# Kernel tuning notes

Measured on AMD Instinct MI355X. Metric: run time of the kernel, lower is better.

Reference implementation:

```python
import jax, jax.numpy as jnp
import numpy as np

B, IMG, C = 128, 128, 3
NP = 8                      # n_patches per side
PS = IMG // NP              # patch size = 16
IN_D = C * PS * PS          # 768
E, NH, L, A = 768, 12, 12, 256
HS = E // NH                # 64
T = NP * NP + 1             # 65 tokens (cls + patches)
LN_EPS = 1e-5


def _pos_emb(seq_len, d):
    i = np.arange(seq_len, dtype=np.float64)[:, None]
    j = np.arange(d, dtype=np.float64)[None, :]
    even = np.sin(i / 10000 ** (j / d))
    odd = np.cos(i / 10000 ** ((j - 1) / d))
    return jnp.asarray(np.where(j % 2 == 0, even, odd), dtype=jnp.float32)


def setup_inputs() -> dict:
    key = jax.random.key(0)
    ks = jax.random.split(key, 16)
    s_e = 1.0 / np.sqrt(E)
    s_in = 1.0 / np.sqrt(IN_D)
    s_4e = 1.0 / np.sqrt(4 * E)
    return {
        "images": jax.random.normal(ks[0], (B, IMG, IMG, C), jnp.float32),
        "lin_w": jax.random.normal(ks[1], (IN_D, E), jnp.float32) * s_in,
        "cls_tok": jax.random.uniform(ks[2], (1, E), jnp.float32),
        "pos_emb": _pos_emb(T, E),
        "Wq": jax.random.normal(ks[3], (L, E, E), jnp.float32) * s_e,
        "Wk": jax.random.normal(ks[4], (L, E, E), jnp.float32) * s_e,
        "Wv": jax.random.normal(ks[5], (L, E, E), jnp.float32) * s_e,
        "Wo": jax.random.normal(ks[6], (L, E, E), jnp.float32) * s_e,
        "bo": jnp.zeros((L, E), jnp.float32),
        "ln1g": jnp.ones((L, E), jnp.float32),
        "ln1b": jnp.zeros((L, E), jnp.float32),
        "ln2g": jnp.ones((L, E), jnp.float32),
        "ln2b": jnp.zeros((L, E), jnp.float32),
        "W1": jax.random.normal(ks[7], (L, E, 4 * E), jnp.float32) * s_e,
        "b1": jnp.zeros((L, 4 * E), jnp.float32),
        "W2": jax.random.normal(ks[8], (L, 4 * E, E), jnp.float32) * s_4e,
        "b2": jnp.zeros((L, E), jnp.float32),
        "head_w": jax.random.normal(ks[9], (E, A), jnp.float32) * s_e,
        "head_b": jnp.zeros((A,), jnp.float32),
    }


def _layernorm(x, g, b):
    mu = jnp.mean(x, axis=-1, keepdims=True)
    var = jnp.var(x, axis=-1, keepdims=True)
    return (x - mu) * jax.lax.rsqrt(var + LN_EPS) * g + b


def _vit_forward(images, lin_w, cls_tok, pos_emb, Wq, Wk, Wv, Wo, bo,
                 ln1g, ln1b, ln2g, ln2b, W1, b1, W2, b2, head_w, head_b):
    n = images.shape[0]
    # patches: 'b (h p1) (w p2) c -> b (h w) (p1 p2 c)'
    p = images.reshape(n, NP, PS, NP, PS, C)
    patches = p.transpose(0, 1, 3, 2, 4, 5).reshape(n, NP * NP, IN_D)
    x = patches @ lin_w                                   # [B, 64, E]
    x = jnp.concatenate([jnp.broadcast_to(cls_tok, (n, 1, E)), x], axis=1)
    x = x + pos_emb[None]                                 # [B, T, E]

    scale = E ** (-0.5)  # NOTE: original scales by n_embd, not head_size

    def block(x, params):
        wq, wk, wv, wo_, bo_, g1, be1, g2, be2, w1, bb1, w2, bb2 = params
        h = _layernorm(x, g1, be1)
        q = (h @ wq).reshape(n, T, NH, HS)
        k = (h @ wk).reshape(n, T, NH, HS)
        v = (h @ wv).reshape(n, T, NH, HS)
        wei = jnp.einsum('bthd,bshd->bhts', q, k) * scale
        wei = jax.nn.softmax(wei, axis=-1)
        attn = jnp.einsum('bhts,bshd->bthd', wei, v).reshape(n, T, E)
        x = x + attn @ wo_ + bo_
        h2 = _layernorm(x, g2, be2)
        x = x + jax.nn.relu(h2 @ w1 + bb1) @ w2 + bb2
        return x, None

    x, _ = jax.lax.scan(block, x,
                        (Wq, Wk, Wv, Wo, bo, ln1g, ln1b, ln2g, ln2b,
                         W1, b1, W2, b2))
    cls = x[:, 0]                                          # [B, E]
    logits = jax.nn.softmax(cls @ head_w + head_b, axis=-1)  # model ends in Softmax
    return logits


def reference(images, lin_w, cls_tok, pos_emb, Wq, Wk, Wv, Wo, bo,
              ln1g, ln1b, ln2g, ln2b, W1, b1, W2, b2, head_w, head_b):
    return _vit_forward(images, lin_w, cls_tok, pos_emb, Wq, Wk, Wv, Wo, bo,
                        ln1g, ln1b, ln2g, ln2b, W1, b1, W2, b2, head_w, head_b)
```

## Files before the change

### kernel.cpp

```cpp
#include <hip/hip_runtime.h>
#include <cstdint>
#include <cstddef>


typedef __bf16 bf16x8 __attribute__((ext_vector_type(8)));
typedef float  f32x4  __attribute__((ext_vector_type(4)));

#define DEVINL __device__ __forceinline__

DEVINL uint16_t f2bf(float f){
  union U{float f; uint32_t i;} v; v.f=f; uint32_t u=v.i;
  return (uint16_t)((u + 0x7fffu + ((u>>16)&1u)) >> 16);
}

DEVINL void gl_lds16(const void* g, void* l){
  __builtin_amdgcn_global_load_lds((const __attribute__((address_space(1))) void*)g,
                                   (__attribute__((address_space(3))) void*)l, 16, 0, 0);
}

__global__ __launch_bounds__(256) void patchify_k(const float* __restrict__ img,
                                                  uint16_t* __restrict__ out){
  int i = blockIdx.x*256 + threadIdx.x;
  int m  = i / 768, kk = i - m*768;
  int b  = m >> 6,  t  = m & 63;
  int py = t >> 3,  px = t & 7;
  int r  = kk / 48, rem = kk - r*48;
  size_t src = ((size_t)(b*128 + py*16 + r)*128 + px*16)*3 + rem;
  out[i] = f2bf(img[src]);
}

DEVINL void tile_transpose(const float* __restrict__ src, uint16_t* __restrict__ dst,
                           int R, int C, int ti, int tj, int tid){
  __shared__ uint16_t tile[32][33];
  int tx = tid & 31, ty = tid >> 5;
  int r0 = ti*32, c0 = tj*32;
  #pragma unroll
  for (int i=0;i<4;++i)
    tile[ty+i*8][tx] = f2bf(src[(size_t)(r0+ty+i*8)*C + c0 + tx]);
  __syncthreads();
  #pragma unroll
  for (int i=0;i<4;++i)
    dst[(size_t)(c0+ty+i*8)*R + r0 + tx] = tile[tx][ty+i*8];
}

__global__ __launch_bounds__(256) void transpose_cvt_k(const float* __restrict__ src,
                                                       uint16_t* __restrict__ dst, int R, int C){
  tile_transpose(src, dst, R, C, blockIdx.y, blockIdx.x, threadIdx.x);
}

__global__ __launch_bounds__(256) void prep_layer_k(
    const float* __restrict__ Wq, const float* __restrict__ Wk,
    const float* __restrict__ Wv, const float* __restrict__ Wo,
    const float* __restrict__ W1, const float* __restrict__ W2,
    uint16_t* __restrict__ wbuf){
  int idx = blockIdx.x;
  const float* src; uint16_t* dst; int R, C, ti, tj;
  if (idx < 2304){
    int m = idx / 576, t = idx - m*576; ti = t/24; tj = t - ti*24; R=768; C=768;
    src = (m==0)?Wq:(m==1)?Wk:(m==2)?Wv:Wo;
    dst = wbuf + (size_t)m*589824;
  } else if (idx < 4608){
    int t = idx - 2304; ti = t/96; tj = t - ti*96; R=768; C=3072;
    src = W1; dst = wbuf + 2359296;
  } else {
    int t = idx - 4608; ti = t/24; tj = t - ti*24; R=3072; C=768;
    src = W2; dst = wbuf + 4718592;
  }
  tile_transpose(src, dst, R, C, ti, tj, threadIdx.x);
}

__global__ __launch_bounds__(256) void cls_init_k(const float* __restrict__ ct,
                                                  const float* __restrict__ pos,
                                                  float* __restrict__ X){
  int b = blockIdx.x, tid = threadIdx.x;
  for (int e = tid; e < 768; e += 256)
    X[(size_t)b*65*768 + e] = ct[e] + pos[e];
}

__global__ __launch_bounds__(256) void ln_k(const float* __restrict__ Xin,
                                            uint16_t* __restrict__ H,
                                            const float* __restrict__ g,
                                            const float* __restrict__ b){
  int row = blockIdx.x, tid = threadIdx.x;
  const float* xr = Xin + (size_t)row*768;
  float v0 = xr[tid], v1 = xr[tid+256], v2 = xr[tid+512];
  int wid = tid>>6, lane = tid&63;
  __shared__ float part[4];
  __shared__ float bc[2];
  float s = v0+v1+v2;
  #pragma unroll
  for (int o=32;o;o>>=1) s += __shfl_down(s,o);
  if (lane==0) part[wid] = s;
  __syncthreads();
  if (tid==0) bc[0] = (part[0]+part[1]+part[2]+part[3]) * (1.f/768.f);
  __syncthreads();
  float mu = bc[0];
  float d0=v0-mu, d1=v1-mu, d2=v2-mu;
  float q = d0*d0 + d1*d1 + d2*d2;
  #pragma unroll
  for (int o=32;o;o>>=1) q += __shfl_down(q,o);
  __syncthreads();
  if (lane==0) part[wid] = q;
  __syncthreads();
  if (tid==0) bc[1] = rsqrtf((part[0]+part[1]+part[2]+part[3])*(1.f/768.f) + 1e-5f);
  __syncthreads();
  float rs = bc[1];
  uint16_t* hr = H + (size_t)row*768;
  hr[tid]     = f2bf(d0*rs*g[tid]     + b[tid]);
  hr[tid+256] = f2bf(d1*rs*g[tid+256] + b[tid+256]);
  hr[tid+512] = f2bf(d2*rs*g[tid+512] + b[tid+512]);
}

enum { EP_BF16=0, EP_RES=1, EP_RELU=2, EP_EMB=3 };

template<int MODE, int BN>
__global__ __launch_bounds__(256) void gemm_bt_k(
    const uint16_t* __restrict__ A, const uint16_t* __restrict__ Bt,
    int M, int N, int K, int strideB, long long strideO,
    const float* __restrict__ bias, float* __restrict__ X,
    uint16_t* __restrict__ Obf, const float* __restrict__ pos)
{
  constexpr int WN = BN/2;
  constexpr int NF = WN/16;
  constexpr int BLOADS = BN/64;
  __shared__ __align__(16) uint16_t sA[3][128*32];
  __shared__ __align__(16) uint16_t sB[3][BN*32];
  const int tid = threadIdx.x;
  const int wid = tid>>6, lane = tid&63;
  const int nx = gridDim.x;
  const int nwg = nx*gridDim.y;
  int idx = blockIdx.y*nx + blockIdx.x;
  int q8 = nwg>>3, r8 = nwg&7, xcd = idx&7, off = idx>>3;
  int swz = (xcd<r8 ? xcd*(q8+1) : r8*(q8+1) + (xcd-r8)*q8) + off;
  const int bn = (swz % nx)*BN, bm = (swz / nx)*128;
  const int z = blockIdx.z;
  const uint16_t* Bz = Bt + (size_t)z*strideB;
  const int wr = wid>>1, wc = wid&1;
  const int frow = lane&15, g = lane>>4;
  int srA[2], scA[2];
  #pragma unroll
  for (int rr=0; rr<2; ++rr){
    int G = rr*256 + tid;
    srA[rr] = G>>2; scA[rr] = ((G&3) - (G>>3)) & 3;
  }
  int srB[BLOADS], scB[BLOADS];
  #pragma unroll
  for (int rr=0; rr<BLOADS; ++rr){
    int G = rr*256 + tid;
    srB[rr] = G>>2; scB[rr] = ((G&3) - (G>>3)) & 3;
  }
  const int rsw = (frow>>1)&3;
  f32x4 acc[4][NF] = {};
  const int nt = K>>5;

  auto stage = [&](char* dA, char* dB, int k0){
    #pragma unroll
    for (int rr=0; rr<2; ++rr)
      gl_lds16(A + (size_t)(bm+srA[rr])*K + k0 + scA[rr]*8, dA + (rr*256 + wid*64)*16);
    #pragma unroll
    for (int rr=0; rr<BLOADS; ++rr)
      gl_lds16(Bz + (size_t)(bn+srB[rr])*K + k0 + scB[rr]*8, dB + (rr*256 + wid*64)*16);
  };

  char *cA=(char*)sA[0], *nA=(char*)sA[1], *fA=(char*)sA[2];
  char *cB=(char*)sB[0], *nB=(char*)sB[1], *fB=(char*)sB[2];
  stage(cA, cB, 0);
  stage(nA, nB, 32);

  for (int t = 0; t < nt; ++t){
    if (t+2 < nt){
      stage(fA, fB, (t+2)<<5);
      if constexpr (BLOADS==1) asm volatile("s_waitcnt vmcnt(6)" ::: "memory");
      else                     asm volatile("s_waitcnt vmcnt(8)" ::: "memory");
    } else if (t+1 < nt){
      if constexpr (BLOADS==1) asm volatile("s_waitcnt vmcnt(3)" ::: "memory");
      else                     asm volatile("s_waitcnt vmcnt(4)" ::: "memory");
    } else {
      asm volatile("s_waitcnt vmcnt(0)" ::: "memory");
    }
    __builtin_amdgcn_s_barrier();
    bf16x8 a[4], b[NF];
    #pragma unroll
    for (int m=0;m<4;++m)
      a[m] = *(const bf16x8*)(cA + (wr*64+m*16+frow)*64 + (((g+rsw)&3)<<4));
    #pragma unroll
    for (int n=0;n<NF;++n)
      b[n] = *(const bf16x8*)(cB + (wc*WN+n*16+frow)*64 + (((g+rsw)&3)<<4));
    #pragma unroll
    for (int m=0;m<4;++m)
      #pragma unroll
      for (int n=0;n<NF;++n)
        acc[m][n] = __builtin_amdgcn_mfma_f32_16x16x32_bf16(a[m], b[n], acc[m][n], 0,0,0);
    __builtin_amdgcn_s_barrier();
    char* t1=cA; cA=nA; nA=fA; fA=t1;
    char* t2=cB; cB=nB; nB=fB; fB=t2;
  }

  uint16_t* Oz = Obf + (size_t)z*(size_t)strideO;
  #pragma unroll
  for (int m=0;m<4;++m){
    int gr0 = bm + wr*64 + m*16 + (lane>>4)*4;
    #pragma unroll
    for (int n=0;n<NF;++n){
      int gc = bn + wc*WN + n*16 + (lane&15);
      #pragma unroll
      for (int r=0;r<4;++r){
        int grow = gr0 + r;
        float vsum = acc[m][n][r];
        if constexpr (MODE==EP_BF16){
          Oz[(size_t)grow*N + gc] = f2bf(vsum);
        } else if constexpr (MODE==EP_RES){
          X[(size_t)grow*N + gc] += vsum + bias[gc];
        } else if constexpr (MODE==EP_RELU){
          float u = vsum + bias[gc];
          Oz[(size_t)grow*N + gc] = f2bf(u > 0.f ? u : 0.f);
        } else {
          int t2i = grow & 63, bb = grow >> 6;
          X[((size_t)bb*65 + 1 + t2i)*768 + gc] = vsum + pos[(size_t)(t2i+1)*768 + gc];
        }
      }
    }
  }
}

__global__ __launch_bounds__(320) void attn_mfma_k(const uint16_t* __restrict__ q,
    const uint16_t* __restrict__ k, const uint16_t* __restrict__ v,
    uint16_t* __restrict__ o)
{
  __shared__ __align__(16) uint16_t P_lds[80][104];
  __shared__ __align__(16) uint16_t Vt[64][104];
  const int bh = blockIdx.x; const int b = bh / 12, hd = bh - b*12;
  const int tid = threadIdx.x;
  const int m = tid>>6;
  const int lane = tid&63;
  const int g = lane>>4, c = lane&15;
  const size_t base = (size_t)b*65*768 + (size_t)hd*64;

  for (int i = tid; i < 80*16; i += 320) P_lds[i>>4][80 + (i&15)] = 0;
  for (int i = tid; i < 64*32; i += 320) Vt[i>>5][64 + (i&31)] = 0;
  __syncthreads();
  for (int j = tid; j < 520; j += 320){
    int key = j >> 3, dc = j & 7;
    union { bf16x8 v8; uint16_t u[8]; } gv;
    gv.v8 = *(const bf16x8*)&v[base + (size_t)key*768 + dc*8];
    #pragma unroll
    for (int e = 0; e < 8; ++e) Vt[dc*8 + e][key] = gv.u[e];
  }

  bf16x8 bk[5][2];
  #pragma unroll
  for (int n=0;n<5;++n)
    #pragma unroll
    for (int kk=0;kk<2;++kk)
      bk[n][kk] = *(const bf16x8*)&k[base + (size_t)(n*16 + c)*768 + kk*32 + g*8];

  bf16x8 aq[2];
  #pragma unroll
  for (int kk=0;kk<2;++kk)
    aq[kk] = *(const bf16x8*)&q[base + (size_t)(m*16 + c)*768 + kk*32 + g*8];
  f32x4 sacc[5] = {};
  #pragma unroll
  for (int kk=0;kk<2;++kk)
    #pragma unroll
    for (int n=0;n<5;++n)
      sacc[n] = __builtin_amdgcn_mfma_f32_16x16x32_bf16(aq[kk], bk[n][kk], sacc[n], 0,0,0);

  const float scale = 0.03608439182435161f;
  #pragma unroll
  for (int r=0;r<4;++r){
    float val[5]; float mx = -3.0e38f;
    #pragma unroll
    for (int n=0;n<5;++n){
      val[n] = (n*16 + c) < 65 ? sacc[n][r]*scale : -3.0e38f;
      mx = fmaxf(mx, val[n]);
    }
    #pragma unroll
    for (int off=1; off<16; off<<=1) mx = fmaxf(mx, __shfl_xor(mx, off));
    float p[5], sum = 0.f;
    #pragma unroll
    for (int n=0;n<5;++n){
      p[n] = (n*16 + c) < 65 ? __expf(val[n]-mx) : 0.f;
      sum += p[n];
    }
    #pragma unroll
    for (int off=1; off<16; off<<=1) sum += __shfl_xor(sum, off);
    float rinv = 1.f / sum;
    int row = m*16 + g*4 + r;
    #pragma unroll
    for (int n=0;n<5;++n) P_lds[row][n*16 + c] = f2bf(p[n]*rinv);
  }
  __syncthreads();

  bf16x8 vb[4][3];
  #pragma unroll
  for (int n=0;n<4;++n)
    #pragma unroll
    for (int kk=0;kk<3;++kk)
      vb[n][kk] = *(const bf16x8*)&Vt[n*16 + c][kk*32 + g*8];
  f32x4 oacc[4] = {};
  #pragma unroll
  for (int kk=0;kk<3;++kk){
    bf16x8 pa = *(const bf16x8*)&P_lds[m*16 + c][kk*32 + g*8];
    #pragma unroll
    for (int n=0;n<4;++n)
      oacc[n] = __builtin_amdgcn_mfma_f32_16x16x32_bf16(pa, vb[n][kk], oacc[n], 0,0,0);
  }
  #pragma unroll
  for (int r=0;r<4;++r){
    int row = m*16 + g*4 + r;
    if (row < 65){
      #pragma unroll
      for (int n=0;n<4;++n)
        o[base + (size_t)row*768 + n*16 + c] = f2bf(oacc[n][r]);
    }
  }
}

__global__ __launch_bounds__(256) void head_k(const float* __restrict__ X,
    const float* __restrict__ W, const float* __restrict__ bias,
    float* __restrict__ out){
  int b = blockIdx.x, a = threadIdx.x;
  const float* xr = X + (size_t)b*65*768;
  float acc = bias[a];
  for (int kk=0; kk<768; ++kk) acc += xr[kk]*W[(size_t)kk*256 + a];
  int wid = a>>6, lane = a&63;
  __shared__ float red[4];
  float mx = acc;
  #pragma unroll
  for (int off=32; off; off>>=1) mx = fmaxf(mx, __shfl_xor(mx, off));
  if (lane==0) red[wid]=mx;
  __syncthreads();
  mx = fmaxf(fmaxf(red[0],red[1]), fmaxf(red[2],red[3]));
  float e = __expf(acc-mx);
  float s = e;
  #pragma unroll
  for (int off=32; off; off>>=1) s += __shfl_xor(s, off);
  __syncthreads();
  if (lane==0) red[wid]=s;
  __syncthreads();
  s = red[0]+red[1]+red[2]+red[3];
  out[(size_t)b*256 + a] = e/s;
}

extern "C" void kernel_launch(void* const* d_in, const int* in_sizes, int n_in,
                              void* d_out, int out_size, void* d_ws, size_t ws_size,
                              hipStream_t stream)
{
  const float* images = (const float*)d_in[0];
  const float* lin_w  = (const float*)d_in[1];
  const float* cls_tok= (const float*)d_in[2];
  const float* pos    = (const float*)d_in[3];
  const float* Wq = (const float*)d_in[4];
  const float* Wk = (const float*)d_in[5];
  const float* Wv = (const float*)d_in[6];
  const float* Wo = (const float*)d_in[7];
  const float* bo = (const float*)d_in[8];
  const float* ln1g=(const float*)d_in[9];
  const float* ln1b=(const float*)d_in[10];
  const float* ln2g=(const float*)d_in[11];
  const float* ln2b=(const float*)d_in[12];
  const float* W1 = (const float*)d_in[13];
  const float* b1 = (const float*)d_in[14];
  const float* W2 = (const float*)d_in[15];
  const float* b2 = (const float*)d_in[16];
  const float* hw = (const float*)d_in[17];
  const float* hb = (const float*)d_in[18];

  char* ws = (char*)d_ws;
  float*    x    = (float*)   (ws + 0);
  uint16_t* h    = (uint16_t*)(ws + 25559040);
  uint16_t* qkv  = (uint16_t*)(ws + 38338560);
  uint16_t* attn = (uint16_t*)(ws + 76677120);
  uint16_t* mid  = (uint16_t*)(ws + 89456640);
  uint16_t* wbuf = (uint16_t*)(ws + 140574720);
  uint16_t* lwt  = (uint16_t*)(ws + 154730496);

  patchify_k<<<24576,256,0,stream>>>(images, mid);
  transpose_cvt_k<<<dim3(24,24),256,0,stream>>>(lin_w, lwt, 768, 768);
  gemm_bt_k<EP_EMB,64><<<dim3(12,64,1),256,0,stream>>>(mid, lwt, 8192,768,768, 0,0,
                                                   nullptr, x, nullptr, pos);
  cls_init_k<<<128,256,0,stream>>>(cls_tok, pos, x);

  for (int l=0;l<12;++l){
    prep_layer_k<<<6912,256,0,stream>>>(Wq+(size_t)l*589824, Wk+(size_t)l*589824,
                                        Wv+(size_t)l*589824, Wo+(size_t)l*589824,
                                        W1+(size_t)l*2359296, W2+(size_t)l*2359296, wbuf);
    ln_k<<<8320,256,0,stream>>>(x, h, ln1g+(size_t)l*768, ln1b+(size_t)l*768);
    gemm_bt_k<EP_BF16,128><<<dim3(6,65,3),256,0,stream>>>(h, wbuf, 8320,768,768,
                                                      589824, 6389760LL,
                                                      nullptr, nullptr, qkv, nullptr);
    attn_mfma_k<<<1536,320,0,stream>>>(qkv, qkv+6389760, qkv+12779520, attn);
    gemm_bt_k<EP_RES,64><<<dim3(12,65,1),256,0,stream>>>(attn, wbuf+1769472, 8320,768,768,
                                                     0,0, bo+(size_t)l*768, x, nullptr, nullptr);
    ln_k<<<8320,256,0,stream>>>(x, h, ln2g+(size_t)l*768, ln2b+(size_t)l*768);
    gemm_bt_k<EP_RELU,128><<<dim3(24,65,1),256,0,stream>>>(h, wbuf+2359296, 8320,3072,768,
                                                       0,0, b1+(size_t)l*3072, nullptr, mid, nullptr);
    gemm_bt_k<EP_RES,64><<<dim3(12,65,1),256,0,stream>>>(mid, wbuf+4718592, 8320,768,3072,
                                                     0,0, b2+(size_t)l*768, x, nullptr, nullptr);
  }
  head_k<<<128,256,0,stream>>>(x, hw, hb, (float*)d_out);
}
```

Before: 3.284 ms.

## Split-K the FFN down-projection and fold partial sums into the next LayerNorm

The W2 GEMM (K=3072) now runs as a 3-way split-K launch with BN=128. Slice 0 adds its result plus bias into the residual. Slices 1 and 2 write fp32 partials into two new buffers that alias workspace regions whose contents are dead at that point. The next layer's LayerNorm (and the final head) sums the residual with both partials and writes the combined value back. The aim is more workgroups and shorter K loops for the deep GEMM, at the cost of extra fp32 partial traffic and a heavier LN kernel.

```diff
diff --git a/kernel.cpp b/kernel.cpp
--- a/kernel.cpp
+++ b/kernel.cpp
@@ -77,13 +77,28 @@
     X[(size_t)b*65*768 + e] = ct[e] + pos[e];
 }
 
+template<int SUM3>
 __global__ __launch_bounds__(256) void ln_k(const float* __restrict__ Xin,
+                                            float* __restrict__ Xout,
+                                            const float* __restrict__ P1,
+                                            const float* __restrict__ P2,
                                             uint16_t* __restrict__ H,
                                             const float* __restrict__ g,
                                             const float* __restrict__ b){
   int row = blockIdx.x, tid = threadIdx.x;
-  const float* xr = Xin + (size_t)row*768;
-  float v0 = xr[tid], v1 = xr[tid+256], v2 = xr[tid+512];
+  const size_t ro = (size_t)row*768;
+  const float* xr = Xin + ro;
+  float v0, v1, v2;
+  if constexpr (SUM3){
+    const float* p1 = P1 + ro; const float* p2 = P2 + ro;
+    v0 = xr[tid]     + p1[tid]     + p2[tid];
+    v1 = xr[tid+256] + p1[tid+256] + p2[tid+256];
+    v2 = xr[tid+512] + p1[tid+512] + p2[tid+512];
+    float* xo = Xout + ro;
+    xo[tid] = v0; xo[tid+256] = v1; xo[tid+512] = v2;
+  } else {
+    v0 = xr[tid]; v1 = xr[tid+256]; v2 = xr[tid+512];
+  }
   int wid = tid>>6, lane = tid&63;
   __shared__ float part[4];
   __shared__ float bc[2];
@@ -105,7 +120,7 @@
   if (tid==0) bc[1] = rsqrtf((part[0]+part[1]+part[2]+part[3])*(1.f/768.f) + 1e-5f);
   __syncthreads();
   float rs = bc[1];
-  uint16_t* hr = H + (size_t)row*768;
+  uint16_t* hr = H + ro;
   hr[tid]     = f2bf(d0*rs*g[tid]     + b[tid]);
   hr[tid+256] = f2bf(d1*rs*g[tid+256] + b[tid+256]);
   hr[tid+512] = f2bf(d2*rs*g[tid+512] + b[tid+512]);
@@ -113,12 +128,13 @@
 
 enum { EP_BF16=0, EP_RES=1, EP_RELU=2, EP_EMB=3 };
 
-template<int MODE, int BN>
+template<int MODE, int BN, int SK>
 __global__ __launch_bounds__(256) void gemm_bt_k(
     const uint16_t* __restrict__ A, const uint16_t* __restrict__ Bt,
     int M, int N, int K, int strideB, long long strideO,
     const float* __restrict__ bias, float* __restrict__ X,
-    uint16_t* __restrict__ Obf, const float* __restrict__ pos)
+    uint16_t* __restrict__ Obf, const float* __restrict__ pos,
+    float* __restrict__ P1, float* __restrict__ P2)
 {
   constexpr int WN = BN/2;
   constexpr int NF = WN/16;
@@ -134,7 +150,9 @@
   int swz = (xcd<r8 ? xcd*(q8+1) : r8*(q8+1) + (xcd-r8)*q8) + off;
   const int bn = (swz % nx)*BN, bm = (swz / nx)*128;
   const int z = blockIdx.z;
-  const uint16_t* Bz = Bt + (size_t)z*strideB;
+  const uint16_t* Bz = (SK==1) ? Bt + (size_t)z*strideB : Bt;
+  const int kbase = (SK==1) ? 0 : z*(K/SK);
+  const int KS = (SK==1) ? K : K/SK;
   const int wr = wid>>1, wc = wid&1;
   const int frow = lane&15, g = lane>>4;
   int srA[2], scA[2];
@@ -151,15 +169,15 @@
   }
   const int rsw = (frow>>1)&3;
   f32x4 acc[4][NF] = {};
-  const int nt = K>>5;
+  const int nt = KS>>5;
 
   auto stage = [&](char* dA, char* dB, int k0){
     #pragma unroll
     for (int rr=0; rr<2; ++rr)
-      gl_lds16(A + (size_t)(bm+srA[rr])*K + k0 + scA[rr]*8, dA + (rr*256 + wid*64)*16);
+      gl_lds16(A + (size_t)(bm+srA[rr])*K + kbase + k0 + scA[rr]*8, dA + (rr*256 + wid*64)*16);
     #pragma unroll
     for (int rr=0; rr<BLOADS; ++rr)
-      gl_lds16(Bz + (size_t)(bn+srB[rr])*K + k0 + scB[rr]*8, dB + (rr*256 + wid*64)*16);
+      gl_lds16(Bz + (size_t)(bn+srB[rr])*K + kbase + k0 + scB[rr]*8, dB + (rr*256 + wid*64)*16);
   };
 
   char *cA=(char*)sA[0], *nA=(char*)sA[1], *fA=(char*)sA[2];
@@ -197,6 +215,7 @@
   }
 
   uint16_t* Oz = Obf + (size_t)z*(size_t)strideO;
+  float* Pz = (SK>1) ? (z==1 ? P1 : P2) : nullptr;
   #pragma unroll
   for (int m=0;m<4;++m){
     int gr0 = bm + wr*64 + m*16 + (lane>>4)*4;
@@ -210,7 +229,12 @@
         if constexpr (MODE==EP_BF16){
           Oz[(size_t)grow*N + gc] = f2bf(vsum);
         } else if constexpr (MODE==EP_RES){
-          X[(size_t)grow*N + gc] += vsum + bias[gc];
+          if constexpr (SK==1){
+            X[(size_t)grow*N + gc] += vsum + bias[gc];
+          } else {
+            if (z==0) X[(size_t)grow*N + gc] += vsum + bias[gc];
+            else      Pz[(size_t)grow*N + gc] = vsum;
+          }
         } else if constexpr (MODE==EP_RELU){
           float u = vsum + bias[gc];
           Oz[(size_t)grow*N + gc] = f2bf(u > 0.f ? u : 0.f);
@@ -317,12 +341,17 @@
 }
 
 __global__ __launch_bounds__(256) void head_k(const float* __restrict__ X,
+    const float* __restrict__ P1, const float* __restrict__ P2,
     const float* __restrict__ W, const float* __restrict__ bias,
     float* __restrict__ out){
   int b = blockIdx.x, a = threadIdx.x;
-  const float* xr = X + (size_t)b*65*768;
+  const size_t ro = (size_t)b*65*768;
+  const float* xr = X + ro;
+  const float* p1 = P1 + ro;
+  const float* p2 = P2 + ro;
   float acc = bias[a];
-  for (int kk=0; kk<768; ++kk) acc += xr[kk]*W[(size_t)kk*256 + a];
+  for (int kk=0; kk<768; ++kk)
+    acc += (xr[kk]+p1[kk]+p2[kk])*W[(size_t)kk*256 + a];
   int wid = a>>6, lane = a&63;
   __shared__ float red[4];
   float mx = acc;
@@ -368,35 +397,43 @@
 
   char* ws = (char*)d_ws;
   float*    x    = (float*)   (ws + 0);
-  uint16_t* h    = (uint16_t*)(ws + 25559040);
+  uint16_t* attn = (uint16_t*)(ws + 25559040);
+  float*    P1   = (float*)   (ws + 25559040);
   uint16_t* qkv  = (uint16_t*)(ws + 38338560);
-  uint16_t* attn = (uint16_t*)(ws + 76677120);
+  float*    P2   = (float*)   (ws + 51118080);
+  uint16_t* h    = (uint16_t*)(ws + 76677120);
   uint16_t* mid  = (uint16_t*)(ws + 89456640);
   uint16_t* wbuf = (uint16_t*)(ws + 140574720);
   uint16_t* lwt  = (uint16_t*)(ws + 154730496);
 
   patchify_k<<<24576,256,0,stream>>>(images, mid);
   transpose_cvt_k<<<dim3(24,24),256,0,stream>>>(lin_w, lwt, 768, 768);
-  gemm_bt_k<EP_EMB,64><<<dim3(12,64,1),256,0,stream>>>(mid, lwt, 8192,768,768, 0,0,
-                                                   nullptr, x, nullptr, pos);
+  gemm_bt_k<EP_EMB,64,1><<<dim3(12,64,1),256,0,stream>>>(mid, lwt, 8192,768,768, 0,0,
+                                                   nullptr, x, nullptr, pos, nullptr, nullptr);
   cls_init_k<<<128,256,0,stream>>>(cls_tok, pos, x);
 
   for (int l=0;l<12;++l){
     prep_layer_k<<<6912,256,0,stream>>>(Wq+(size_t)l*589824, Wk+(size_t)l*589824,
                                         Wv+(size_t)l*589824, Wo+(size_t)l*589824,
                                         W1+(size_t)l*2359296, W2+(size_t)l*2359296, wbuf);
-    ln_k<<<8320,256,0,stream>>>(x, h, ln1g+(size_t)l*768, ln1b+(size_t)l*768);
-    gemm_bt_k<EP_BF16,128><<<dim3(6,65,3),256,0,stream>>>(h, wbuf, 8320,768,768,
+    if (l==0)
+      ln_k<0><<<8320,256,0,stream>>>(x, nullptr, nullptr, nullptr, h,
+                                     ln1g, ln1b);
+    else
+      ln_k<1><<<8320,256,0,stream>>>(x, x, P1, P2, h,
+                                     ln1g+(size_t)l*768, ln1b+(size_t)l*768);
+    gemm_bt_k<EP_BF16,128,1><<<dim3(6,65,3),256,0,stream>>>(h, wbuf, 8320,768,768,
                                                       589824, 6389760LL,
-                                                      nullptr, nullptr, qkv, nullptr);
+                                                      nullptr, nullptr, qkv, nullptr, nullptr, nullptr);
     attn_mfma_k<<<1536,320,0,stream>>>(qkv, qkv+6389760, qkv+12779520, attn);
-    gemm_bt_k<EP_RES,64><<<dim3(12,65,1),256,0,stream>>>(attn, wbuf+1769472, 8320,768,768,
-                                                     0,0, bo+(size_t)l*768, x, nullptr, nullptr);
-    ln_k<<<8320,256,0,stream>>>(x, h, ln2g+(size_t)l*768, ln2b+(size_t)l*768);
-    gemm_bt_k<EP_RELU,128><<<dim3(24,65,1),256,0,stream>>>(h, wbuf+2359296, 8320,3072,768,
-                                                       0,0, b1+(size_t)l*3072, nullptr, mid, nullptr);
-    gemm_bt_k<EP_RES,64><<<dim3(12,65,1),256,0,stream>>>(mid, wbuf+4718592, 8320,768,3072,
-                                                     0,0, b2+(size_t)l*768, x, nullptr, nullptr);
-  }
-  head_k<<<128,256,0,stream>>>(x, hw, hb, (float*)d_out);
-}
+    gemm_bt_k<EP_RES,64,1><<<dim3(12,65,1),256,0,stream>>>(attn, wbuf+1769472, 8320,768,768,
+                                                     0,0, bo+(size_t)l*768, x, nullptr, nullptr, nullptr, nullptr);
+    ln_k<0><<<8320,256,0,stream>>>(x, nullptr, nullptr, nullptr, h,
+                                   ln2g+(size_t)l*768, ln2b+(size_t)l*768);
+    gemm_bt_k<EP_RELU,128,1><<<dim3(24,65,1),256,0,stream>>>(h, wbuf+2359296, 8320,3072,768,
+                                                       0,0, b1+(size_t)l*3072, nullptr, mid, nullptr, nullptr, nullptr);
+    gemm_bt_k<EP_RES,128,3><<<dim3(6,65,3),256,0,stream>>>(mid, wbuf+4718592, 8320,768,3072,
+                                                     0,0, b2+(size_t)l*768, x, nullptr, nullptr, P1, P2);
+  }
+  head_k<<<128,256,0,stream>>>(x, P1, P2, hw, hb, (float*)d_out);
+}
```

After: 3.304 ms. No clear change (+0.6%).

## Add 256x128 MFMA GEMM with split-K W2 and fold partial residual into LN

Applied to the files above, without the earlier changes.

Adds a new 512-thread GEMM kernel with 256x128 block tiles, double-buffered direct-to-LDS loads, swizzled LDS reads and XCD-aware block remapping. It replaces the QKV, W1 and W2 GEMMs. The W2 GEMM is split into two K halves: one half adds into the residual stream, and the other writes a float partial buffer that aliases the attention workspace. The next layer's first LayerNorm, or the head, adds that partial back in. The aim is more data reuse per tile and more parallelism on the long-K GEMM, at the cost of extra partial-buffer traffic and tighter workspace aliasing.

```diff
diff --git a/kernel.cpp b/kernel.cpp
--- a/kernel.cpp
+++ b/kernel.cpp
@@ -77,13 +77,27 @@
     X[(size_t)b*65*768 + e] = ct[e] + pos[e];
 }
 
+template<int SUMP>
 __global__ __launch_bounds__(256) void ln_k(const float* __restrict__ Xin,
+                                            float* __restrict__ Xout,
+                                            const float* __restrict__ P1,
                                             uint16_t* __restrict__ H,
                                             const float* __restrict__ g,
                                             const float* __restrict__ b){
   int row = blockIdx.x, tid = threadIdx.x;
-  const float* xr = Xin + (size_t)row*768;
-  float v0 = xr[tid], v1 = xr[tid+256], v2 = xr[tid+512];
+  const size_t ro = (size_t)row*768;
+  const float* xr = Xin + ro;
+  float v0, v1, v2;
+  if constexpr (SUMP){
+    const float* p1 = P1 + ro;
+    v0 = xr[tid]     + p1[tid];
+    v1 = xr[tid+256] + p1[tid+256];
+    v2 = xr[tid+512] + p1[tid+512];
+    float* xo = Xout + ro;
+    xo[tid] = v0; xo[tid+256] = v1; xo[tid+512] = v2;
+  } else {
+    v0 = xr[tid]; v1 = xr[tid+256]; v2 = xr[tid+512];
+  }
   int wid = tid>>6, lane = tid&63;
   __shared__ float part[4];
   __shared__ float bc[2];
@@ -105,7 +119,7 @@
   if (tid==0) bc[1] = rsqrtf((part[0]+part[1]+part[2]+part[3])*(1.f/768.f) + 1e-5f);
   __syncthreads();
   float rs = bc[1];
-  uint16_t* hr = H + (size_t)row*768;
+  uint16_t* hr = H + ro;
   hr[tid]     = f2bf(d0*rs*g[tid]     + b[tid]);
   hr[tid+256] = f2bf(d1*rs*g[tid+256] + b[tid+256]);
   hr[tid+512] = f2bf(d2*rs*g[tid+512] + b[tid+512]);
@@ -223,6 +237,108 @@
   }
 }
 
+template<int MODE, int SK>
+__global__ __launch_bounds__(512) void gemm2m_k(
+    const uint16_t* __restrict__ A, const uint16_t* __restrict__ Bt,
+    int M, int N, int K, int strideB, long long strideO,
+    const float* __restrict__ bias, float* __restrict__ X,
+    uint16_t* __restrict__ Obf, float* __restrict__ P1)
+{
+  __shared__ __align__(16) uint16_t sA[2][256*32];
+  __shared__ __align__(16) uint16_t sB[2][128*32];
+  const int tid = threadIdx.x;
+  const int wid = tid>>6, lane = tid&63;
+  const int nx = gridDim.x;
+  const int nwg = nx*gridDim.y;
+  int idx = blockIdx.y*nx + blockIdx.x;
+  int q8 = nwg>>3, r8 = nwg&7, xcd = idx&7, off = idx>>3;
+  int swz = (xcd<r8 ? xcd*(q8+1) : r8*(q8+1) + (xcd-r8)*q8) + off;
+  const int bn = (swz % nx)*128, bm = (swz / nx)*256;
+  const int z = blockIdx.z;
+  const uint16_t* Bz = (SK==1) ? Bt + (size_t)z*strideB : Bt;
+  const int kbase = (SK==1) ? 0 : z*(K/SK);
+  const int KS = (SK==1) ? K : K/SK;
+  const int wr = wid>>1, wc = wid&1;
+  const int frow = lane&15, g = lane>>4;
+  int srA[2], scA[2];
+  #pragma unroll
+  for (int rr=0; rr<2; ++rr){
+    int G = rr*512 + tid;
+    srA[rr] = G>>2; scA[rr] = ((G&3) - (G>>3)) & 3;
+  }
+  const int srB = tid>>2, scB = ((tid&3) - (tid>>3)) & 3;
+  const int rsw = (frow>>1)&3;
+  f32x4 acc[4][4] = {};
+  const int nt = KS>>5;
+
+  auto stage = [&](int bsel, int k0){
+    char* dA = (char*)sA[bsel]; char* dB = (char*)sB[bsel];
+    #pragma unroll
+    for (int rr=0; rr<2; ++rr)
+      gl_lds16(A + (size_t)(bm+srA[rr])*K + kbase + k0 + scA[rr]*8,
+               dA + (rr*512 + wid*64)*16);
+    gl_lds16(Bz + (size_t)(bn+srB)*K + kbase + k0 + scB*8, dB + (wid*64)*16);
+  };
+
+  stage(0, 0);
+  int buf = 0;
+  for (int t = 0; t < nt; ++t){
+    if (t+1 < nt){
+      stage(buf^1, (t+1)<<5);
+      asm volatile("s_waitcnt vmcnt(3)" ::: "memory");
+    } else {
+      asm volatile("s_waitcnt vmcnt(0)" ::: "memory");
+    }
+    __builtin_amdgcn_s_barrier();
+    const char* sAc = (const char*)sA[buf];
+    const char* sBc = (const char*)sB[buf];
+    bf16x8 a[4], b[4];
+    #pragma unroll
+    for (int m=0;m<4;++m)
+      a[m] = *(const bf16x8*)(sAc + (wr*64+m*16+frow)*64 + (((g+rsw)&3)<<4));
+    #pragma unroll
+    for (int n=0;n<4;++n)
+      b[n] = *(const bf16x8*)(sBc + (wc*64+n*16+frow)*64 + (((g+rsw)&3)<<4));
+    #pragma unroll
+    for (int m=0;m<4;++m)
+      #pragma unroll
+      for (int n=0;n<4;++n)
+        acc[m][n] = __builtin_amdgcn_mfma_f32_16x16x32_bf16(a[m], b[n], acc[m][n], 0,0,0);
+    __builtin_amdgcn_s_barrier();
+    buf ^= 1;
+  }
+
+  uint16_t* Oz = Obf + (size_t)z*(size_t)strideO;
+  #pragma unroll
+  for (int m=0;m<4;++m){
+    int gr0 = bm + wr*64 + m*16 + (lane>>4)*4;
+    #pragma unroll
+    for (int n=0;n<4;++n){
+      int gc = bn + wc*64 + n*16 + (lane&15);
+      #pragma unroll
+      for (int r=0;r<4;++r){
+        int grow = gr0 + r;
+        if (grow < M){
+          float vsum = acc[m][n][r];
+          if constexpr (MODE==EP_BF16){
+            Oz[(size_t)grow*N + gc] = f2bf(vsum);
+          } else if constexpr (MODE==EP_RES){
+            if constexpr (SK==1){
+              X[(size_t)grow*N + gc] += vsum + bias[gc];
+            } else {
+              if (z==0) X[(size_t)grow*N + gc] += vsum + bias[gc];
+              else      P1[(size_t)grow*N + gc] = vsum;
+            }
+          } else if constexpr (MODE==EP_RELU){
+            float u = vsum + bias[gc];
+            Oz[(size_t)grow*N + gc] = f2bf(u > 0.f ? u : 0.f);
+          }
+        }
+      }
+    }
+  }
+}
+
 __global__ __launch_bounds__(320) void attn_mfma_k(const uint16_t* __restrict__ q,
     const uint16_t* __restrict__ k, const uint16_t* __restrict__ v,
     uint16_t* __restrict__ o)
@@ -317,12 +433,16 @@
 }
 
 __global__ __launch_bounds__(256) void head_k(const float* __restrict__ X,
+    const float* __restrict__ P1,
     const float* __restrict__ W, const float* __restrict__ bias,
     float* __restrict__ out){
   int b = blockIdx.x, a = threadIdx.x;
-  const float* xr = X + (size_t)b*65*768;
+  const size_t ro = (size_t)b*65*768;
+  const float* xr = X + ro;
+  const float* p1 = P1 + ro;
   float acc = bias[a];
-  for (int kk=0; kk<768; ++kk) acc += xr[kk]*W[(size_t)kk*256 + a];
+  for (int kk=0; kk<768; ++kk)
+    acc += (xr[kk]+p1[kk])*W[(size_t)kk*256 + a];
   int wid = a>>6, lane = a&63;
   __shared__ float red[4];
   float mx = acc;
@@ -368,9 +488,10 @@
 
   char* ws = (char*)d_ws;
   float*    x    = (float*)   (ws + 0);
-  uint16_t* h    = (uint16_t*)(ws + 25559040);
+  uint16_t* attn = (uint16_t*)(ws + 25559040);
+  float*    P1   = (float*)   (ws + 25559040);
   uint16_t* qkv  = (uint16_t*)(ws + 38338560);
-  uint16_t* attn = (uint16_t*)(ws + 76677120);
+  uint16_t* h    = (uint16_t*)(ws + 76677120);
   uint16_t* mid  = (uint16_t*)(ws + 89456640);
   uint16_t* wbuf = (uint16_t*)(ws + 140574720);
   uint16_t* lwt  = (uint16_t*)(ws + 154730496);
@@ -385,18 +506,23 @@
     prep_layer_k<<<6912,256,0,stream>>>(Wq+(size_t)l*589824, Wk+(size_t)l*589824,
                                         Wv+(size_t)l*589824, Wo+(size_t)l*589824,
                                         W1+(size_t)l*2359296, W2+(size_t)l*2359296, wbuf);
-    ln_k<<<8320,256,0,stream>>>(x, h, ln1g+(size_t)l*768, ln1b+(size_t)l*768);
-    gemm_bt_k<EP_BF16,128><<<dim3(6,65,3),256,0,stream>>>(h, wbuf, 8320,768,768,
-                                                      589824, 6389760LL,
-                                                      nullptr, nullptr, qkv, nullptr);
+    if (l==0)
+      ln_k<0><<<8320,256,0,stream>>>(x, nullptr, nullptr, h, ln1g, ln1b);
+    else
+      ln_k<1><<<8320,256,0,stream>>>(x, x, P1, h,
+                                     ln1g+(size_t)l*768, ln1b+(size_t)l*768);
+    gemm2m_k<EP_BF16,1><<<dim3(6,33,3),512,0,stream>>>(h, wbuf, 8320,768,768,
+                                                       589824, 6389760LL,
+                                                       nullptr, nullptr, qkv, nullptr);
     attn_mfma_k<<<1536,320,0,stream>>>(qkv, qkv+6389760, qkv+12779520, attn);
     gemm_bt_k<EP_RES,64><<<dim3(12,65,1),256,0,stream>>>(attn, wbuf+1769472, 8320,768,768,
                                                      0,0, bo+(size_t)l*768, x, nullptr, nullptr);
-    ln_k<<<8320,256,0,stream>>>(x, h, ln2g+(size_t)l*768, ln2b+(size_t)l*768);
-    gemm_bt_k<EP_RELU,128><<<dim3(24,65,1),256,0,stream>>>(h, wbuf+2359296, 8320,3072,768,
-                                                       0,0, b1+(size_t)l*3072, nullptr, mid, nullptr);
-    gemm_bt_k<EP_RES,64><<<dim3(12,65,1),256,0,stream>>>(mid, wbuf+4718592, 8320,768,3072,
-                                                     0,0, b2+(size_t)l*768, x, nullptr, nullptr);
-  }
-  head_k<<<128,256,0,stream>>>(x, hw, hb, (float*)d_out);
-}
+    ln_k<0><<<8320,256,0,stream>>>(x, nullptr, nullptr, h,
+                                   ln2g+(size_t)l*768, ln2b+(size_t)l*768);
+    gemm2m_k<EP_RELU,1><<<dim3(24,33,1),512,0,stream>>>(h, wbuf+2359296, 8320,3072,768,
+                                                        0,0, b1+(size_t)l*3072, nullptr, mid, nullptr);
+    gemm2m_k<EP_RES,2><<<dim3(6,33,2),512,0,stream>>>(mid, wbuf+4718592, 8320,768,3072,
+                                                      0,0, b2+(size_t)l*768, x, nullptr, P1);
+  }
+  head_k<<<128,256,0,stream>>>(x, P1, hw, hb, (float*)d_out);
+}
```

Measured after the change: 3.140 ms. 1.05x faster.
